# Performance work log

Hardware: AMD Instinct MI355X
Metric: run time of the kernel (lower is better)

## Reference

```python
import jax, jax.numpy as jnp
import numpy as np
from jax import lax

GROUPS = 4
KH = KW = 3
K = KH * KW
STRIDE = (1, 1)
PAD = ((1, 1), (1, 1))
DIL = (1, 1)


def _bilinear_gather(padded, py, px):
    # padded: (B,C,Hp,Wp); py,px: (B,C,K,Ho,Wo) float sample positions in padded coords
    B, C, Hp, Wp = padded.shape
    bi = jnp.arange(B)[:, None, None, None, None]
    ci = jnp.arange(C)[None, :, None, None, None]
    y0 = jnp.floor(py)
    x0 = jnp.floor(px)
    wy = py - y0
    wx = px - x0
    out = jnp.zeros(py.shape, padded.dtype)
    corners = ((0, 0, (1 - wy) * (1 - wx)), (0, 1, (1 - wy) * wx),
               (1, 0, wy * (1 - wx)), (1, 1, wy * wx))
    for dy, dx, w in corners:
        yy = y0 + dy
        xx = x0 + dx
        valid = (yy >= 0) & (yy < Hp) & (xx >= 0) & (xx < Wp)  # zero outside (implicit zero padding)
        yc = jnp.clip(yy, 0, Hp - 1).astype(jnp.int32)
        xc = jnp.clip(xx, 0, Wp - 1).astype(jnp.int32)
        out = out + jnp.where(valid, padded[bi, ci, yc, xc] * w, 0.0)
    return out


def deform_conv2d(inps, weight, bias, weight_off, bias_off):
    B, C, H, W = inps.shape
    # offset/mask predicting conv (grouped, same geometry as the main conv)
    off = lax.conv_general_dilated(inps, weight_off, STRIDE, PAD, rhs_dilation=DIL,
                                   feature_group_count=GROUPS,
                                   dimension_numbers=('NCHW', 'OIHW', 'NCHW'))
    off = off + bias_off[None, :, None, None]
    Ho, Wo = off.shape[2], off.shape[3]
    off = off.reshape(B, 3, C * K, Ho, Wo)  # (B, dim+1, C*K, Ho, Wo)
    dy = off[:, 0].reshape(B, C, K, Ho, Wo)
    dx = off[:, 1].reshape(B, C, K, Ho, Wo)
    # softmax across the GROUP axis, as in the original reshape(b,1,groups,-1,h,w).softmax(dim=2)
    mask = jax.nn.softmax(off[:, 2].reshape(B, GROUPS, (C // GROUPS) * K, Ho, Wo), axis=1)
    mask = mask.reshape(B, C, K, Ho, Wo)

    padded = jnp.pad(inps, ((0, 0), (0, 0), PAD[0], PAD[1]))
    ky, kx = jnp.meshgrid(jnp.arange(KH), jnp.arange(KW), indexing='ij')
    ky = ky.ravel().astype(inps.dtype)
    kx = kx.ravel().astype(inps.dtype)
    oh = jnp.arange(Ho, dtype=inps.dtype)
    ow = jnp.arange(Wo, dtype=inps.dtype)
    # sample position per (batch, in-channel, kernel tap, output pixel)
    py = oh[None, None, None, :, None] * STRIDE[0] + ky[None, None, :, None, None] * DIL[0] + dy
    px = ow[None, None, None, None, :] * STRIDE[1] + kx[None, None, :, None, None] * DIL[1] + dx

    sampled = _bilinear_gather(padded, py, px) * mask  # (B,C,K,Ho,Wo)

    Cout = weight.shape[0]
    Cg = C // GROUPS
    wg = weight.reshape(GROUPS, Cout // GROUPS, Cg, K)          # (g, o, c, k)
    sg = sampled.reshape(B, GROUPS, Cg, K, Ho, Wo)              # (b, g, c, k, h, w)
    out = jnp.einsum('bgckhw,gock->bgohw', sg, wg).reshape(B, Cout, Ho, Wo)
    return out + bias[None, :, None, None]


def setup_inputs() -> dict:
    key = jax.random.key(0)
    k0, k1, k2, k3 = jax.random.split(key, 4)
    B, C, H, W = 8, 64, 64, 64
    Cout = 64
    inps = jax.random.normal(k0, (B, C, H, W), dtype=jnp.float32)
    weight = jax.random.normal(k1, (Cout, C // GROUPS, KH, KW), dtype=jnp.float32) * 0.05
    bias = jax.random.normal(k2, (Cout,), dtype=jnp.float32) * 0.05
    # small offset-conv weights -> offsets of a few pixels, non-saturated softmax
    weight_off = jax.random.normal(k3, (C * K * 3, C // GROUPS, KH, KW), dtype=jnp.float32) * 0.05
    bias_off = jnp.zeros((C * K * 3,), dtype=jnp.float32)
    return {'inps': inps, 'weight': weight, 'bias': bias,
            'weight_off': weight_off, 'bias_off': bias_off}


def reference(inps, weight, bias, weight_off, bias_off):
    return deform_conv2d(inps, weight, bias, weight_off, bias_off)
```

## Files before the change

### kernel.cpp

```cpp
#include <hip/hip_runtime.h>

typedef __attribute__((ext_vector_type(8))) short short8;
typedef __attribute__((ext_vector_type(4))) float f32x4;

__device__ __forceinline__ unsigned short bf16rne(float f) {
    unsigned u = __float_as_uint(f);
    u += 0x7FFFu + ((u >> 16) & 1u);
    return (unsigned short)(u >> 16);
}
__device__ __forceinline__ float bf16dec(unsigned short h) {
    return __uint_as_float((unsigned)h << 16);
}
__device__ __forceinline__ unsigned cvtpk2(float lo, float hi) {
    unsigned r;
    asm("v_cvt_pk_bf16_f32 %0, %1, %2" : "=v"(r) : "v"(lo), "v"(hi));
    return r;
}
__device__ __forceinline__ unsigned short cvt1(float f) {
    return (unsigned short)cvtpk2(f, f);
}
__device__ __forceinline__ float declo(unsigned u) { return __uint_as_float(u << 16); }
__device__ __forceinline__ float dechi(unsigned u) { return __uint_as_float(u & 0xFFFF0000u); }

extern __shared__ char smem[];


#define IMC8_OFF   0
#define PATCH8_OFF 37376
#define SX8_OFF    62720
#define LGX8_OFF   72960
#define LDS_V8     81664
#define OTB8_OFF   37376

#define LOG2E 1.4426950408889634f

#define PWOFF_U32  138240
#define PWM_U32    5120
#define WS_NEEDED  ((size_t)(PWOFF_U32 + PWM_U32) * 4)

__global__ __launch_bounds__(256)
void pack_weights(const float* __restrict__ wmain,
                  const float* __restrict__ woff,
                  unsigned* __restrict__ pw)
{
    int idx = blockIdx.x * 256 + threadIdx.x;
    if (idx < PWOFF_U32) {
        int j2   = idx & 3;
        int lane = (idx >> 2) & 63;
        int rest = idx >> 8;
        int kt   = rest % 5;
        int t    = rest / 5;
        int comp = t / 36, r36 = t - comp * 36;
        int jw   = r36 / 9, ntg = r36 - jw * 9;
        int ochb = comp * 576 + jw * 144 + ntg * 16;
        int g    = ochb / 432;
        int ktf  = (9 * g) >> 1;
        int och  = ochb + (lane & 15);
        int ck   = (ktf + kt) * 32 + (lane >> 4) * 8 + j2 * 2 - g * 144;
        float v0 = 0.f, v1 = 0.f;
        if ((unsigned)ck < 144u)       v0 = woff[(size_t)och * 144 + ck];
        if ((unsigned)(ck + 1) < 144u) v1 = woff[(size_t)och * 144 + ck + 1];
        pw[idx] = (unsigned)bf16rne(v0) | ((unsigned)bf16rne(v1) << 16);
    } else if (idx < PWOFF_U32 + PWM_U32) {
        int m    = idx - PWOFF_U32;
        int j2   = m & 3;
        int lane = (m >> 2) & 63;
        int rest = m >> 8;
        int jw   = rest / 5, pair = rest - jw * 5;
        int och  = jw * 16 + (lane & 15);
        int w0   = pair * 32 + (lane >> 4) * 8 + j2 * 2;
        float v0 = (w0 < 144)     ? wmain[(size_t)och * 144 + w0]     : 0.f;
        float v1 = (w0 + 1 < 144) ? wmain[(size_t)och * 144 + w0 + 1] : 0.f;
        pw[idx] = (unsigned)bf16rne(v0) | ((unsigned)bf16rne(v1) << 16);
    }
}

__global__ __launch_bounds__(512, 4)
void deform_v8(const float* __restrict__ inps,
               const float* __restrict__ bmain,
               const float* __restrict__ boff,
               const unsigned short* __restrict__ pwoff,
               const unsigned short* __restrict__ pwm,
               float* __restrict__ out)
{
    unsigned short* IMC   = (unsigned short*)(smem + IMC8_OFF);
    unsigned short* PATCH = (unsigned short*)(smem + PATCH8_OFF);
    unsigned short* SX    = (unsigned short*)(smem + SX8_OFF);
    unsigned short* LGX   = (unsigned short*)(smem + LGX8_OFF);
    float*          OTB   = (float*)(smem + OTB8_OFF);

    const int tid  = threadIdx.x;
    const int lane = tid & 63;
    const int wv   = __builtin_amdgcn_readfirstlane(tid >> 6);
    const int jw   = wv & 3;
    const int mtw  = wv >> 2;
    const int slot = lane & 15;
    const int q    = lane >> 4;

    const int b    = blockIdx.x >> 7;
    const int tile = blockIdx.x & 127;
    const int ty0  = (tile >> 3) << 2;
    const int tx0  = (tile & 7) << 3;

    const float* inb = inps + (size_t)b * 262144;

    for (int e = tid; e < 12288; e += 512) {
        int c = e / 192, rem = e - c * 192;
        int y = rem >> 4, x = rem & 15;
        int gy = ty0 + y - 4, gx = tx0 + x - 4;
        float v = 0.f;
        if ((unsigned)gy < 64u && (unsigned)gx < 64u)
            v = inb[(c * 64 + gy) * 64 + gx];
        PATCH[c * 198 + rem] = cvt1(v);
    }
    __syncthreads();

    {
        const int px  = tid >> 4;
        const int sub = tid & 15;
        const int pyr = px >> 3, pxx = px & 7;
        unsigned* dst = (unsigned*)(IMC + px * 584);
        #pragma unroll 3
        for (int i = 0; i < 18; ++i) {
            int u  = i * 16 + sub;
            int kk = u * 2;
            int c0 = kk / 9,        r0 = kk - c0 * 9;
            int c1 = (kk + 1) / 9,  r1 = (kk + 1) - c1 * 9;
            unsigned short a  = PATCH[c0 * 198 + (pyr + r0 / 3 + 3) * 16 + pxx + r0 % 3 + 3];
            unsigned short bb = PATCH[c1 * 198 + (pyr + r1 / 3 + 3) * 16 + pxx + r1 % 3 + 3];
            dst[u] = (unsigned)a | ((unsigned)bb << 16);
        }
    }
    __syncthreads();

    f32x4 aco = {0.f, 0.f, 0.f, 0.f};

    auto pair_mfma = [&](int pair) {
        const short8 bfr = ((const short8*)pwm)[(jw * 5 + pair) * 64 + lane];
        const short8 a8  = *(const short8*)(SX + jw * 1280 + (mtw * 16 + slot) * 40 + q * 8);
        aco = __builtin_amdgcn_mfma_f32_16x16x32_bf16(a8, bfr, aco, 0, 0, 0);
    };

    for (int ntg = 0; ntg < 9; ++ntg) {
        const int lb = (ntg & 1) * 2176;

        short8 bwA[15];
        #pragma unroll
        for (int comp = 0; comp < 3; ++comp) {
            const short8* wp = (const short8*)pwoff + (comp * 36 + jw * 9 + ntg) * 320 + lane;
            #pragma unroll
            for (int kt = 0; kt < 5; ++kt) bwA[comp * 5 + kt] = wp[kt * 64];
        }

        f32x4 aD = {0.f,0.f,0.f,0.f};
        f32x4 aX = {0.f,0.f,0.f,0.f};
        f32x4 aM = {0.f,0.f,0.f,0.f};

        auto gemm3 = [&](f32x4& acc, int comp) {
            const int ochb = comp * 576 + jw * 144 + ntg * 16;
            const int g    = ochb / 432;
            const int ktf  = (9 * g) >> 1;
            const short8* ap0 = (const short8*)(smem + IMC8_OFF);
            #pragma unroll
            for (int kt = 0; kt < 5; ++kt) {
                const short8 af = ap0[(mtw * 16 + slot) * 73 + (ktf + kt) * 4 + q];
                acc = __builtin_amdgcn_mfma_f32_16x16x32_bf16(af, bwA[comp * 5 + kt], acc, 0, 0, 0);
            }
            const float bo = boff[ochb + slot];
            acc[0] += bo; acc[1] += bo; acc[2] += bo; acc[3] += bo;
        };
        gemm3(aD, 0); gemm3(aX, 1); gemm3(aM, 2);

        float er[4];
        #pragma unroll
        for (int r = 0; r < 4; ++r) {
            er[r] = exp2f(aM[r] * LOG2E);
            int pxr = mtw * 16 + q * 4 + r;
            LGX[lb + pxr * 68 + slot * 4 + jw] = cvt1(er[r]);
        }
        __syncthreads();

        const int rr  = ntg * 16 + slot;
        const int cg  = rr / 9;
        const int kk9 = rr - cg * 9;
        const int kyk = kk9 / 3, kxk = kk9 - kyk * 3;
        const int c   = jw * 16 + cg;
        const float* inc = inb + c * 4096;
        const int pbase = c * 198;
        const int par = ntg & 1;
        const float fyk = (float)(ty0 + kyk - 1);
        const float fxk = (float)(tx0 + kxk - 1);

        #pragma unroll
        for (int r = 0; r < 4; ++r) {
            const int pxr = mtw * 16 + q * 4 + r;
            const int pyr = pxr >> 3, pxx = pxr & 7;

            const uint2 lg = *(const uint2*)(LGX + lb + pxr * 68 + slot * 4);
            const float s4 = declo(lg.x) + dechi(lg.x) + declo(lg.y) + dechi(lg.y);
            const float msk = er[r] / s4;

            float pyf = fyk + (float)pyr + aD[r];
            float pxf = fxk + (float)pxx + aX[r];
            float y0f = floorf(pyf), x0f = floorf(pxf);
            float wy = pyf - y0f, wx = pxf - x0f;
            int iy0 = (int)y0f, ix0 = (int)x0f;

            int ly0 = iy0 - ty0 + 4;
            int lx0 = ix0 - tx0 + 4;
            float v;
            if ((unsigned)ly0 < 11u && (unsigned)lx0 < 15u) {
                const int a = pbase + ly0 * 16 + lx0;
                float p00 = bf16dec(PATCH[a]),      p01 = bf16dec(PATCH[a + 1]);
                float p10 = bf16dec(PATCH[a + 16]), p11 = bf16dec(PATCH[a + 17]);
                float top = fmaf(wx, p01 - p00, p00);
                float bot = fmaf(wx, p11 - p10, p10);
                v = fmaf(wy, bot - top, top);
            } else {
                float w00 = (1.f - wy) * (1.f - wx), w01 = (1.f - wy) * wx;
                float w10 = wy * (1.f - wx),         w11 = wy * wx;
                v = 0.f;
                if ((unsigned)iy0 < 64u) {
                    if ((unsigned)ix0 < 64u)       v += w00 * inc[iy0 * 64 + ix0];
                    if ((unsigned)(ix0 + 1) < 64u) v += w01 * inc[iy0 * 64 + ix0 + 1];
                }
                if ((unsigned)(iy0 + 1) < 64u) {
                    if ((unsigned)ix0 < 64u)       v += w10 * inc[(iy0 + 1) * 64 + ix0];
                    if ((unsigned)(ix0 + 1) < 64u) v += w11 * inc[(iy0 + 1) * 64 + ix0 + 1];
                }
            }
            SX[jw * 1280 + pxr * 40 + par * 16 + slot] = cvt1(v * msk);
        }

        if (ntg & 1)  { asm volatile("" ::: "memory"); pair_mfma(ntg >> 1); }
        if (ntg == 8) { asm volatile("" ::: "memory"); pair_mfma(4); }
    }
    __syncthreads();

    {
        const int o = jw * 16 + slot;
        const float bo = bmain[o];
        #pragma unroll
        for (int r = 0; r < 4; ++r)
            OTB[o * 33 + mtw * 16 + q * 4 + r] = aco[r] + bo;
    }
    __syncthreads();
    #pragma unroll
    for (int i = 0; i < 4; ++i) {
        int f  = i * 512 + tid;
        int oo = f >> 5, pp = f & 31;
        out[(size_t)(b * 64 + oo) * 4096 + (ty0 + (pp >> 3)) * 64 + (tx0 + (pp & 7))] =
            OTB[oo * 33 + pp];
    }
}

#define V2IMC_OFF   0
#define V2S_OFF     37376
#define V2LGX_OFF   74752
#define V2LDS_BYTES 78848

__global__ __launch_bounds__(256, 2)
void deform_v2(const float* __restrict__ inps,
               const float* __restrict__ wmain,
               const float* __restrict__ bmain,
               const float* __restrict__ woff,
               const float* __restrict__ boff,
               float* __restrict__ out)
{
    unsigned short* IMC  = (unsigned short*)(smem + V2IMC_OFF);
    unsigned short* SBUF = (unsigned short*)(smem + V2S_OFF);
    unsigned short* LGX  = (unsigned short*)(smem + V2LGX_OFF);
    float* PATCH = (float*)(smem + V2S_OFF);
    float* OTB   = (float*)(smem + V2IMC_OFF);

    const int tid  = threadIdx.x;
    const int lane = tid & 63;
    const int jw   = __builtin_amdgcn_readfirstlane(tid >> 6);
    const int slot = lane & 15;
    const int q    = lane >> 4;

    const int b    = blockIdx.x >> 7;
    const int tile = blockIdx.x & 127;
    const int ty0  = (tile >> 3) << 2;
    const int tx0  = (tile & 7) << 3;

    const float* inb = inps + (size_t)b * 262144;

    for (int e = tid; e < 64 * 60; e += 256) {
        int ch = e / 60, rem = e - ch * 60;
        int iy = rem / 10, ix = rem - iy * 10;
        int gy = ty0 + iy - 1, gx = tx0 + ix - 1;
        float v = 0.f;
        if ((unsigned)gy < 64u && (unsigned)gx < 64u)
            v = inb[(ch * 64 + gy) * 64 + gx];
        PATCH[ch * 61 + rem] = v;
    }
    __syncthreads();
    {
        const int px  = tid >> 3;
        const int sub = tid & 7;
        const int pyr = px >> 3, pxx = px & 7;
        unsigned short* dst = IMC + px * 584;
        for (int i = 0; i < 36; ++i) {
            int kk = sub * 72 + 2 * i;
            float v0, v1;
            { int c = kk / 9, r9 = kk - c * 9, ky = r9 / 3, kx = r9 - ky * 3;
              v0 = PATCH[c * 61 + (pyr + ky) * 10 + (pxx + kx)]; }
            { int k1 = kk + 1; int c = k1 / 9, r9 = k1 - c * 9, ky = r9 / 3, kx = r9 - ky * 3;
              v1 = PATCH[c * 61 + (pyr + ky) * 10 + (pxx + kx)]; }
            *(unsigned*)(dst + kk) = cvtpk2(v0, v1);
        }
    }
    __syncthreads();

    for (int ntg = 0; ntg < 9; ++ntg) {
        f32x4 aD[2] = {{0.f,0.f,0.f,0.f},{0.f,0.f,0.f,0.f}};
        f32x4 aX[2] = {{0.f,0.f,0.f,0.f},{0.f,0.f,0.f,0.f}};
        f32x4 aM[2] = {{0.f,0.f,0.f,0.f},{0.f,0.f,0.f,0.f}};

        auto gemm3 = [&](f32x4* acc, int comp) {
            const int ochb = comp * 576 + jw * 144 + ntg * 16;
            const int g    = ochb / 432;
            const int ktf  = (9 * g) >> 1;
            const int ch0  = g * 18;
            const int och  = ochb + slot;
            #pragma unroll
            for (int kt = 0; kt < 5; ++kt) {
                const int ktg   = ktf + kt;
                const int chunk = ktg * 4 + q;
                short8 bfr;
                if ((unsigned)(chunk - ch0) < 18u) {
                    const float4* wp = (const float4*)(woff + (size_t)och * 144 + (chunk - ch0) * 8);
                    float4 w0 = wp[0], w1 = wp[1];
                    union { unsigned u[4]; short8 s; } cv;
                    cv.u[0] = cvtpk2(w0.x, w0.y); cv.u[1] = cvtpk2(w0.z, w0.w);
                    cv.u[2] = cvtpk2(w1.x, w1.y); cv.u[3] = cvtpk2(w1.z, w1.w);
                    bfr = cv.s;
                } else {
                    bfr = short8{0,0,0,0,0,0,0,0};
                }
                #pragma unroll
                for (int mt = 0; mt < 2; ++mt) {
                    const short8* ap = (const short8*)(smem + V2IMC_OFF +
                                        (mt * 16 + slot) * 1168 + ktg * 64 + q * 16);
                    acc[mt] = __builtin_amdgcn_mfma_f32_16x16x32_bf16(*ap, bfr, acc[mt], 0, 0, 0);
                }
            }
            const float bo = boff[ochb + slot];
            #pragma unroll
            for (int mt = 0; mt < 2; ++mt) {
                acc[mt][0] += bo; acc[mt][1] += bo; acc[mt][2] += bo; acc[mt][3] += bo;
            }
        };
        gemm3(aD, 0); gemm3(aX, 1); gemm3(aM, 2);

        #pragma unroll
        for (int mt = 0; mt < 2; ++mt)
        #pragma unroll
        for (int r = 0; r < 4; ++r) {
            int pxr = mt * 16 + q * 4 + r;
            LGX[(jw * 32 + pxr) * 16 + slot] = bf16rne(aM[mt][r]);
        }
        __syncthreads();

        const int rr  = ntg * 16 + slot;
        const int cg  = rr / 9;
        const int kk9 = rr - cg * 9;
        const int kyk = kk9 / 3, kxk = kk9 - kyk * 3;
        const float* inc = inb + (jw * 16 + cg) * 4096;

        #pragma unroll
        for (int mt = 0; mt < 2; ++mt)
        #pragma unroll
        for (int r = 0; r < 4; ++r) {
            const int pxr = mt * 16 + q * 4 + r;
            const int pyr = pxr >> 3, pxx = pxr & 7;
            float own = aM[mt][r];
            float l0 = (jw == 0) ? own : bf16dec(LGX[(0 * 32 + pxr) * 16 + slot]);
            float l1 = (jw == 1) ? own : bf16dec(LGX[(1 * 32 + pxr) * 16 + slot]);
            float l2 = (jw == 2) ? own : bf16dec(LGX[(2 * 32 + pxr) * 16 + slot]);
            float l3 = (jw == 3) ? own : bf16dec(LGX[(3 * 32 + pxr) * 16 + slot]);
            float m4 = fmaxf(fmaxf(l0, l1), fmaxf(l2, l3));
            float s4 = __expf(l0 - m4) + __expf(l1 - m4) + __expf(l2 - m4) + __expf(l3 - m4);
            float msk = __expf(own - m4) / s4;

            float pyf = (float)(ty0 + pyr + kyk - 1) + aD[mt][r];
            float pxf = (float)(tx0 + pxx + kxk - 1) + aX[mt][r];
            float y0f = floorf(pyf), x0f = floorf(pxf);
            float wy = pyf - y0f, wx = pxf - x0f;
            int iy0 = (int)y0f, ix0 = (int)x0f;
            float w00 = (1.f - wy) * (1.f - wx), w01 = (1.f - wy) * wx;
            float w10 = wy * (1.f - wx),         w11 = wy * wx;
            float v = 0.f;
            if ((unsigned)iy0 < 64u) {
                if ((unsigned)ix0 < 64u)       v += w00 * inc[iy0 * 64 + ix0];
                if ((unsigned)(ix0 + 1) < 64u) v += w01 * inc[iy0 * 64 + ix0 + 1];
            }
            if ((unsigned)(iy0 + 1) < 64u) {
                if ((unsigned)ix0 < 64u)       v += w10 * inc[(iy0 + 1) * 64 + ix0];
                if ((unsigned)(ix0 + 1) < 64u) v += w11 * inc[(iy0 + 1) * 64 + ix0 + 1];
            }
            SBUF[pxr * 584 + jw * 144 + rr] = bf16rne(v * msk);
        }
        __syncthreads();
    }

    {
        f32x4 aco2[2] = {{0.f,0.f,0.f,0.f},{0.f,0.f,0.f,0.f}};
        const int ktf = (9 * jw) >> 1;
        const int ch0 = jw * 18;
        const int o   = jw * 16 + slot;
        #pragma unroll
        for (int kt = 0; kt < 5; ++kt) {
            const int ktg   = ktf + kt;
            const int chunk = ktg * 4 + q;
            short8 bfr;
            if ((unsigned)(chunk - ch0) < 18u) {
                const float4* wp = (const float4*)(wmain + (size_t)o * 144 + (chunk - ch0) * 8);
                float4 w0 = wp[0], w1 = wp[1];
                union { unsigned u[4]; short8 s; } cv;
                cv.u[0] = cvtpk2(w0.x, w0.y); cv.u[1] = cvtpk2(w0.z, w0.w);
                cv.u[2] = cvtpk2(w1.x, w1.y); cv.u[3] = cvtpk2(w1.z, w1.w);
                bfr = cv.s;
            } else {
                bfr = short8{0,0,0,0,0,0,0,0};
            }
            #pragma unroll
            for (int mt = 0; mt < 2; ++mt) {
                const short8* ap = (const short8*)(smem + V2S_OFF +
                                    (mt * 16 + slot) * 1168 + ktg * 64 + q * 16);
                aco2[mt] = __builtin_amdgcn_mfma_f32_16x16x32_bf16(*ap, bfr, aco2[mt], 0, 0, 0);
            }
        }
        const float bo = bmain[o];
        __syncthreads();
        #pragma unroll
        for (int mt = 0; mt < 2; ++mt)
        #pragma unroll
        for (int r = 0; r < 4; ++r)
            OTB[o * 33 + mt * 16 + q * 4 + r] = aco2[mt][r] + bo;
    }
    __syncthreads();
    #pragma unroll
    for (int i = 0; i < 8; ++i) {
        int f  = i * 256 + tid;
        int oo = f >> 5, pp = f & 31;
        out[(size_t)(b * 64 + oo) * 4096 + (ty0 + (pp >> 3)) * 64 + (tx0 + (pp & 7))] =
            OTB[oo * 33 + pp];
    }
}

extern "C" void kernel_launch(void* const* d_in, const int* in_sizes, int n_in,
                              void* d_out, int out_size, void* d_ws, size_t ws_size,
                              hipStream_t stream) {
    const float* inps   = (const float*)d_in[0];
    const float* weight = (const float*)d_in[1];
    const float* bias   = (const float*)d_in[2];
    const float* woff   = (const float*)d_in[3];
    const float* boff   = (const float*)d_in[4];
    float* outp = (float*)d_out;

    if (ws_size >= WS_NEEDED) {
        unsigned* pw = (unsigned*)d_ws;
        pack_weights<<<dim3(560), dim3(256), 0, stream>>>(weight, woff, pw);
        hipFuncSetAttribute((const void*)deform_v8,
                            hipFuncAttributeMaxDynamicSharedMemorySize, LDS_V8);
        deform_v8<<<dim3(1024), dim3(512), LDS_V8, stream>>>(
            inps, bias, boff,
            (const unsigned short*)pw,
            (const unsigned short*)(pw + PWOFF_U32), outp);
    } else {
        hipFuncSetAttribute((const void*)deform_v2,
                            hipFuncAttributeMaxDynamicSharedMemorySize, V2LDS_BYTES);
        deform_v2<<<dim3(1024), dim3(256), V2LDS_BYTES, stream>>>(
            inps, weight, bias, woff, boff, outp);
    }
}
```

Baseline: 123.8 us.

## Remap offset-conv channels so group softmax reduces in-register via DPP

Reassigns output channels to lanes so the four group members of each softmax sit in adjacent lanes. The softmax denominator is then computed with DPP swizzles instead of going through an LDS staging buffer and an extra barrier per iteration. The offset weights are now packed as plain row-major bf16, and B fragments are gathered per lane with masking across an 18-step K loop. This issues more MFMAs per iteration, including zero-padded ones, and makes the weight loads less coalesced, in exchange for fewer LDS round-trips. The main-conv weights are repacked to match the new SX layout.

```diff
diff --git a/kernel.cpp b/kernel.cpp
--- a/kernel.cpp
+++ b/kernel.cpp
@@ -19,24 +19,21 @@
 __device__ __forceinline__ unsigned short cvt1(float f) {
     return (unsigned short)cvtpk2(f, f);
 }
-__device__ __forceinline__ float declo(unsigned u) { return __uint_as_float(u << 16); }
-__device__ __forceinline__ float dechi(unsigned u) { return __uint_as_float(u & 0xFFFF0000u); }
 
 extern __shared__ char smem[];
 
 
-#define IMC8_OFF   0
-#define PATCH8_OFF 37376
-#define SX8_OFF    62720
-#define LGX8_OFF   72960
-#define LDS_V8     81664
-#define OTB8_OFF   37376
+#define IMC9_OFF   0
+#define PATCH9_OFF 37376
+#define SX9_OFF    62720
+#define LDS_V9     81280
+#define OTB9_OFF   37376
 
 #define LOG2E 1.4426950408889634f
 
-#define PWOFF_U32  138240
-#define PWM_U32    5120
-#define WS_NEEDED  ((size_t)(PWOFF_U32 + PWM_U32) * 4)
+#define PW2_U32   124416
+#define PWM_U32   5120
+#define WS_NEEDED ((size_t)(PW2_U32 + PWM_U32) * 4)
 
 __global__ __launch_bounds__(256)
 void pack_weights(const float* __restrict__ wmain,
@@ -44,58 +41,51 @@
                   unsigned* __restrict__ pw)
 {
     int idx = blockIdx.x * 256 + threadIdx.x;
-    if (idx < PWOFF_U32) {
-        int j2   = idx & 3;
-        int lane = (idx >> 2) & 63;
-        int rest = idx >> 8;
-        int kt   = rest % 5;
-        int t    = rest / 5;
-        int comp = t / 36, r36 = t - comp * 36;
-        int jw   = r36 / 9, ntg = r36 - jw * 9;
-        int ochb = comp * 576 + jw * 144 + ntg * 16;
-        int g    = ochb / 432;
-        int ktf  = (9 * g) >> 1;
-        int och  = ochb + (lane & 15);
-        int ck   = (ktf + kt) * 32 + (lane >> 4) * 8 + j2 * 2 - g * 144;
-        float v0 = 0.f, v1 = 0.f;
-        if ((unsigned)ck < 144u)       v0 = woff[(size_t)och * 144 + ck];
-        if ((unsigned)(ck + 1) < 144u) v1 = woff[(size_t)och * 144 + ck + 1];
+    if (idx < PW2_U32) {
+        int och = idx / 72, c2 = (idx - och * 72) * 2;
+        float v0 = woff[(size_t)och * 144 + c2];
+        float v1 = woff[(size_t)och * 144 + c2 + 1];
         pw[idx] = (unsigned)bf16rne(v0) | ((unsigned)bf16rne(v1) << 16);
-    } else if (idx < PWOFF_U32 + PWM_U32) {
-        int m    = idx - PWOFF_U32;
+    } else if (idx < PW2_U32 + PWM_U32) {
+        int m    = idx - PW2_U32;
         int j2   = m & 3;
         int lane = (m >> 2) & 63;
         int rest = m >> 8;
-        int jw   = rest / 5, pair = rest - jw * 5;
-        int och  = jw * 16 + (lane & 15);
-        int w0   = pair * 32 + (lane >> 4) * 8 + j2 * 2;
-        float v0 = (w0 < 144)     ? wmain[(size_t)och * 144 + w0]     : 0.f;
-        float v1 = (w0 + 1 < 144) ? wmain[(size_t)och * 144 + w0 + 1] : 0.f;
+        int j_o  = rest / 5, kt2 = rest - j_o * 5;
+        int o    = j_o * 16 + (lane & 15);
+        int kk2  = kt2 * 32 + (lane >> 4) * 8 + j2 * 2;
+        float v0 = 0.f, v1 = 0.f;
+        if (kk2 < 144)     v0 = wmain[(size_t)o * 144 + (kk2 & 15) * 9 + (kk2 >> 4)];
+        if (kk2 + 1 < 144) v1 = wmain[(size_t)o * 144 + ((kk2 + 1) & 15) * 9 + ((kk2 + 1) >> 4)];
         pw[idx] = (unsigned)bf16rne(v0) | ((unsigned)bf16rne(v1) << 16);
     }
 }
 
 __global__ __launch_bounds__(512, 4)
-void deform_v8(const float* __restrict__ inps,
+void deform_v9(const float* __restrict__ inps,
                const float* __restrict__ bmain,
                const float* __restrict__ boff,
-               const unsigned short* __restrict__ pwoff,
+               const unsigned short* __restrict__ pw2,
                const unsigned short* __restrict__ pwm,
                float* __restrict__ out)
 {
-    unsigned short* IMC   = (unsigned short*)(smem + IMC8_OFF);
-    unsigned short* PATCH = (unsigned short*)(smem + PATCH8_OFF);
-    unsigned short* SX    = (unsigned short*)(smem + SX8_OFF);
-    unsigned short* LGX   = (unsigned short*)(smem + LGX8_OFF);
-    float*          OTB   = (float*)(smem + OTB8_OFF);
+    unsigned short* IMC   = (unsigned short*)(smem + IMC9_OFF);
+    unsigned short* PATCH = (unsigned short*)(smem + PATCH9_OFF);
+    unsigned short* SX    = (unsigned short*)(smem + SX9_OFF);
+    float*          OTB   = (float*)(smem + OTB9_OFF);
 
     const int tid  = threadIdx.x;
     const int lane = tid & 63;
     const int wv   = __builtin_amdgcn_readfirstlane(tid >> 6);
-    const int jw   = wv & 3;
+    const int ws4  = wv & 3;
     const int mtw  = wv >> 2;
     const int slot = lane & 15;
     const int q    = lane >> 4;
+
+    const int j_s  = slot & 3;
+    const int cgi  = slot >> 2;
+    const int cg_s = ws4 * 4 + cgi;
+    const int c_s  = j_s * 16 + cg_s;
 
     const int b    = blockIdx.x >> 7;
     const int tile = blockIdx.x & 127;
@@ -133,72 +123,89 @@
     }
     __syncthreads();
 
+    int dbs0, dbs1, dbs2;
+    {
+        int g0 = (0 * 576 + c_s * 9) / 432;
+        int g1 = (1 * 576 + c_s * 9) / 432;
+        int g2 = (2 * 576 + c_s * 9) / 432;
+        dbs0 = q * 8 - g0 * 144;
+        dbs1 = q * 8 - g1 * 144;
+        dbs2 = q * 8 - g2 * 144;
+    }
+
     f32x4 aco = {0.f, 0.f, 0.f, 0.f};
-
-    auto pair_mfma = [&](int pair) {
-        const short8 bfr = ((const short8*)pwm)[(jw * 5 + pair) * 64 + lane];
-        const short8 a8  = *(const short8*)(SX + jw * 1280 + (mtw * 16 + slot) * 40 + q * 8);
+    auto pair_mfma = [&](int kt2) {
+        const short8 bfr = ((const short8*)pwm)[(ws4 * 5 + kt2) * 64 + lane];
+        const short8 a8  = *(const short8*)(SX + ws4 * 2320 + (mtw * 16 + slot) * 72
+                                            + (kt2 & 1) * 32 + q * 8);
         aco = __builtin_amdgcn_mfma_f32_16x16x32_bf16(a8, bfr, aco, 0, 0, 0);
     };
 
-    for (int ntg = 0; ntg < 9; ++ntg) {
-        const int lb = (ntg & 1) * 2176;
-
-        short8 bwA[15];
-        #pragma unroll
-        for (int comp = 0; comp < 3; ++comp) {
-            const short8* wp = (const short8*)pwoff + (comp * 36 + jw * 9 + ntg) * 320 + lane;
-            #pragma unroll
-            for (int kt = 0; kt < 5; ++kt) bwA[comp * 5 + kt] = wp[kt * 64];
-        }
+    const short8* ap = (const short8*)(smem + IMC9_OFF) + (mtw * 16 + slot) * 73 + q;
+
+    for (int k = 0; k < 9; ++k) {
+        const int och_s = c_s * 9 + k;
+        const unsigned short* rpa0 = pw2 + och_s * 144 + dbs0;
+        const unsigned short* rpa1 = pw2 + (576 * 1 + och_s) * 144 + dbs1;
+        const unsigned short* rpa2 = pw2 + (576 * 2 + och_s) * 144 + dbs2;
 
         f32x4 aD = {0.f,0.f,0.f,0.f};
         f32x4 aX = {0.f,0.f,0.f,0.f};
         f32x4 aM = {0.f,0.f,0.f,0.f};
 
-        auto gemm3 = [&](f32x4& acc, int comp) {
-            const int ochb = comp * 576 + jw * 144 + ntg * 16;
-            const int g    = ochb / 432;
-            const int ktf  = (9 * g) >> 1;
-            const short8* ap0 = (const short8*)(smem + IMC8_OFF);
+        #pragma unroll
+        for (int ktg = 0; ktg < 18; ++ktg) {
+            const short8 af = ap[ktg * 4];
+            if (ktg <= 8) {
+                short8 bfr = {0,0,0,0,0,0,0,0};
+                if ((unsigned)(ktg * 32 + dbs0) < 144u)
+                    bfr = *(const short8*)(rpa0 + ktg * 32);
+                aD = __builtin_amdgcn_mfma_f32_16x16x32_bf16(af, bfr, aD, 0, 0, 0);
+            }
+            if (ktg >= 4 && ktg <= 13) {
+                short8 bfr = {0,0,0,0,0,0,0,0};
+                if ((unsigned)(ktg * 32 + dbs1) < 144u)
+                    bfr = *(const short8*)(rpa1 + ktg * 32);
+                aX = __builtin_amdgcn_mfma_f32_16x16x32_bf16(af, bfr, aX, 0, 0, 0);
+            }
+            if (ktg >= 9) {
+                short8 bfr = {0,0,0,0,0,0,0,0};
+                if ((unsigned)(ktg * 32 + dbs2) < 144u)
+                    bfr = *(const short8*)(rpa2 + ktg * 32);
+                aM = __builtin_amdgcn_mfma_f32_16x16x32_bf16(af, bfr, aM, 0, 0, 0);
+            }
+        }
+        {
+            const float b0 = boff[och_s];
+            const float b1 = boff[576 + och_s];
+            const float b2 = boff[1152 + och_s];
             #pragma unroll
-            for (int kt = 0; kt < 5; ++kt) {
-                const short8 af = ap0[(mtw * 16 + slot) * 73 + (ktf + kt) * 4 + q];
-                acc = __builtin_amdgcn_mfma_f32_16x16x32_bf16(af, bwA[comp * 5 + kt], acc, 0, 0, 0);
-            }
-            const float bo = boff[ochb + slot];
-            acc[0] += bo; acc[1] += bo; acc[2] += bo; acc[3] += bo;
-        };
-        gemm3(aD, 0); gemm3(aX, 1); gemm3(aM, 2);
+            for (int i = 0; i < 4; ++i) { aD[i] += b0; aX[i] += b1; aM[i] += b2; }
+        }
 
         float er[4];
         #pragma unroll
         for (int r = 0; r < 4; ++r) {
-            er[r] = exp2f(aM[r] * LOG2E);
-            int pxr = mtw * 16 + q * 4 + r;
-            LGX[lb + pxr * 68 + slot * 4 + jw] = cvt1(er[r]);
-        }
-        __syncthreads();
-
-        const int rr  = ntg * 16 + slot;
-        const int cg  = rr / 9;
-        const int kk9 = rr - cg * 9;
-        const int kyk = kk9 / 3, kxk = kk9 - kyk * 3;
-        const int c   = jw * 16 + cg;
-        const float* inc = inb + c * 4096;
-        const int pbase = c * 198;
-        const int par = ntg & 1;
+            float e  = exp2f(aM[r] * LOG2E);
+            float e1 = __int_as_float(__builtin_amdgcn_mov_dpp(
+                           __float_as_int(e), 0xB1, 0xF, 0xF, true));
+            float s2 = e + e1;
+            float s3 = __int_as_float(__builtin_amdgcn_mov_dpp(
+                           __float_as_int(s2), 0x4E, 0xF, 0xF, true));
+            er[r] = e * __builtin_amdgcn_rcpf(s2 + s3);
+        }
+
+        const int kyk = k / 3, kxk = k - kyk * 3;
         const float fyk = (float)(ty0 + kyk - 1);
         const float fxk = (float)(tx0 + kxk - 1);
+        const float* inc = inb + c_s * 4096;
+        const int pbase = c_s * 198;
+        const int sxb = j_s * 2320 + ((k >> 1) & 1) * 32 + (k & 1) * 16 + cg_s;
 
         #pragma unroll
         for (int r = 0; r < 4; ++r) {
             const int pxr = mtw * 16 + q * 4 + r;
             const int pyr = pxr >> 3, pxx = pxr & 7;
-
-            const uint2 lg = *(const uint2*)(LGX + lb + pxr * 68 + slot * 4);
-            const float s4 = declo(lg.x) + dechi(lg.x) + declo(lg.y) + dechi(lg.y);
-            const float msk = er[r] / s4;
 
             float pyf = fyk + (float)pyr + aD[r];
             float pxf = fxk + (float)pxx + aX[r];
@@ -229,16 +236,16 @@
                     if ((unsigned)(ix0 + 1) < 64u) v += w11 * inc[(iy0 + 1) * 64 + ix0 + 1];
                 }
             }
-            SX[jw * 1280 + pxr * 40 + par * 16 + slot] = cvt1(v * msk);
-        }
-
-        if (ntg & 1)  { asm volatile("" ::: "memory"); pair_mfma(ntg >> 1); }
-        if (ntg == 8) { asm volatile("" ::: "memory"); pair_mfma(4); }
-    }
-    __syncthreads();
+            SX[sxb + pxr * 72] = cvt1(v * er[r]);
+        }
+
+        if (k & 1) { __syncthreads(); pair_mfma(k >> 1); }
+    }
+    __syncthreads();
+    pair_mfma(4);
 
     {
-        const int o = jw * 16 + slot;
+        const int o = ws4 * 16 + slot;
         const float bo = bmain[o];
         #pragma unroll
         for (int r = 0; r < 4; ++r)
@@ -462,13 +469,13 @@
 
     if (ws_size >= WS_NEEDED) {
         unsigned* pw = (unsigned*)d_ws;
-        pack_weights<<<dim3(560), dim3(256), 0, stream>>>(weight, woff, pw);
-        hipFuncSetAttribute((const void*)deform_v8,
-                            hipFuncAttributeMaxDynamicSharedMemorySize, LDS_V8);
-        deform_v8<<<dim3(1024), dim3(512), LDS_V8, stream>>>(
+        pack_weights<<<dim3(507), dim3(256), 0, stream>>>(weight, woff, pw);
+        hipFuncSetAttribute((const void*)deform_v9,
+                            hipFuncAttributeMaxDynamicSharedMemorySize, LDS_V9);
+        deform_v9<<<dim3(1024), dim3(512), LDS_V9, stream>>>(
             inps, bias, boff,
             (const unsigned short*)pw,
-            (const unsigned short*)(pw + PWOFF_U32), outp);
+            (const unsigned short*)(pw + PW2_U32), outp);
     } else {
         hipFuncSetAttribute((const void*)deform_v2,
                             hipFuncAttributeMaxDynamicSharedMemorySize, V2LDS_BYTES);
```

Measured after the change: 221.7 us. 1.79x slower.
